# Performance work log

Hardware: AMD Instinct MI355X
Metric: run time of the kernel (lower is better)

Reference implementation:

```python
import jax, jax.numpy as jnp
import numpy as np

TEMP = 13.544
EPS = 1e-5  # BatchNorm2d default eps


def setup_inputs() -> dict:
    key = jax.random.key(0)
    k1, = jax.random.split(key, 1)
    N, S, E = 16, 1024, 512
    x = jax.random.normal(k1, (N, S, E), dtype=jnp.float32)
    gamma = jnp.ones((1,), dtype=jnp.float32)   # BatchNorm2d(1).weight
    beta = jnp.zeros((1,), dtype=jnp.float32)   # BatchNorm2d(1).bias
    return {"x": x, "gamma": gamma, "beta": beta}


def reference(x, gamma, beta):
    # Pairwise squared L2 distances via GEMM identity:
    # ||a-b||^2 = ||a||^2 + ||b||^2 - 2 a.b   (symmetric, matches the
    # original broadcast diff+square+sum without the O(S^2 E) intermediate)
    sq = jnp.sum(x * x, axis=-1)                    # (N, S)
    gram = jnp.einsum('bse,bte->bst', x, x)         # (N, S, S)
    d = sq[:, :, None] + sq[:, None, :] - 2.0 * gram  # (N, S, S)
    d = jnp.maximum(d, 0.0)                          # numerical floor (exact math is >= 0)

    # BatchNorm2d(1) in training mode: stats over all elements of the single channel
    d = d[:, None, :, :]                             # (N, 1, S, S)
    mean = jnp.mean(d)
    var = jnp.mean((d - mean) ** 2)                  # biased variance, as torch uses for normalization
    d_hat = (d - mean) * jax.lax.rsqrt(var + EPS)
    out = d_hat * gamma.reshape(1, 1, 1, 1) + beta.reshape(1, 1, 1, 1)

    # softmax(-out / 13.544) over last dim
    return jax.nn.softmax(-out / TEMP, axis=-1)      # (N, 1, S, S)
```

## Files before the change

kernel.cpp:

```cpp
#include <hip/hip_runtime.h>
#include <hip/hip_bf16.h>


#define S_DIM 1024
#define E_DIM 512
#define NBATCH 16
#define NSTEP (E_DIM / 32)
#define TEMP_C 13.544

typedef __attribute__((ext_vector_type(4))) float f32x4;
typedef __attribute__((ext_vector_type(8))) short bf16x8;
typedef __attribute__((ext_vector_type(8))) _Float16 f16x8;

__device__ inline unsigned pkbf(float lo, float hi) {
  unsigned a = __float_as_uint(lo), b = __float_as_uint(hi);
  a = (a + 0x7FFFu + ((a >> 16) & 1u)) >> 16;
  b = (b + 0x7FFFu + ((b >> 16) & 1u)) & 0xFFFF0000u;
  return b | a;
}

__device__ inline void gload16(const void* g, void* l) {
  __builtin_amdgcn_global_load_lds(
      (const __attribute__((address_space(1))) unsigned*)g,
      (__attribute__((address_space(3))) unsigned*)l, 16, 0, 0);
}

__global__ __launch_bounds__(256) void sqcvt(const float* __restrict__ x,
                                             ushort* __restrict__ xb16,
                                             float* __restrict__ sq,
                                             double* __restrict__ sums) {
  const int wave = threadIdx.x >> 6, lane = threadIdx.x & 63;
  const size_t row = (size_t)blockIdx.x * 4 + wave;
  const float4* xr = reinterpret_cast<const float4*>(x + row * E_DIM);
  float4 a = xr[lane * 2], b = xr[lane * 2 + 1];
  uint4 p;
  p.x = pkbf(a.x, a.y); p.y = pkbf(a.z, a.w);
  p.z = pkbf(b.x, b.y); p.w = pkbf(b.z, b.w);
  *reinterpret_cast<uint4*>(xb16 + row * E_DIM + lane * 8) = p;
  float s = a.x*a.x + a.y*a.y + a.z*a.z + a.w*a.w +
            b.x*b.x + b.y*b.y + b.z*b.z + b.w*b.w;
#pragma unroll
  for (int o = 32; o > 0; o >>= 1) s += __shfl_xor(s, o);
  if (lane == 0) sq[row] = s;
  if (blockIdx.x == 0 && threadIdx.x == 0) { sums[0] = 0.0; sums[1] = 0.0; }
}

template <int MODE>
__global__ __launch_bounds__(512, 2) void gram5(const ushort* __restrict__ xb16,
                                                const float* __restrict__ sq,
                                                float* __restrict__ dout,
                                                _Float16* __restrict__ dp,
                                                double* __restrict__ sums) {
  __shared__ ushort lA[3][8192];
  __shared__ ushort lB[3][8192];
  __shared__ double red[16];

  const int tid = threadIdx.x, wave = tid >> 6, lane = tid & 63;
  const int wr = wave >> 2, wc = wave & 3;

  const int bid = blockIdx.x;
  const int xcd = bid & 7, j = bid >> 3;
  const int b = xcd * 2 + (j >> 4);
  const int tile = j & 15;
  const int tr = tile >> 2, tc = tile & 3;

  const ushort* xb = xb16 + (size_t)b * (S_DIM * E_DIM);
  const int rowA0 = tr * 256, rowB0 = tc * 256;

  int eA[2], eB[2];
#pragma unroll
  for (int i = 0; i < 2; ++i) {
    int p = i * 512 + tid;
    int r = p >> 2;
    int s = (p & 3) ^ ((r >> 1) & 3);
    eA[i] = (rowA0 + r) * E_DIM + s * 8;
    eB[i] = (rowB0 + r) * E_DIM + s * 8;
  }

  auto stage = [&](int buf, int k0) {
    char* la = (char*)&lA[buf][0];
    char* lb = (char*)&lB[buf][0];
    gload16(xb + eA[0] + k0, la + (wave * 64 + lane) * 16);
    gload16(xb + eA[1] + k0, la + 8192 + (wave * 64 + lane) * 16);
    gload16(xb + eB[0] + k0, lb + (wave * 64 + lane) * 16);
    gload16(xb + eB[1] + k0, lb + 8192 + (wave * 64 + lane) * 16);
  };

  f32x4 acc[8][4] = {};

  stage(0, 0);
  stage(1, 32);
  int cur = 0;
#pragma unroll 1
  for (int ks = 0; ks < NSTEP; ++ks) {
    if (ks < NSTEP - 1) {
      asm volatile("s_waitcnt vmcnt(4)" ::: "memory");
    } else {
      asm volatile("s_waitcnt vmcnt(0)" ::: "memory");
    }
    __builtin_amdgcn_s_barrier();
    __builtin_amdgcn_sched_barrier(0);
    if (ks + 2 < NSTEP) {
      int nb = cur + 2; if (nb >= 3) nb -= 3;
      stage(nb, (ks + 2) * 32);
    }
    __builtin_amdgcn_sched_barrier(0);

    bf16x8 af[8], bfr[4];
    const int s0 = lane >> 4;
    const char* la = (const char*)&lA[cur][0];
    const char* lb = (const char*)&lB[cur][0];
#pragma unroll
    for (int m = 0; m < 8; ++m) {
      int row = wr * 128 + m * 16 + (lane & 15);
      af[m] = *reinterpret_cast<const bf16x8*>(la + row * 64 + ((s0 ^ ((row >> 1) & 3)) << 4));
    }
#pragma unroll
    for (int n = 0; n < 4; ++n) {
      int row = wc * 64 + n * 16 + (lane & 15);
      bfr[n] = *reinterpret_cast<const bf16x8*>(lb + row * 64 + ((s0 ^ ((row >> 1) & 3)) << 4));
    }
#pragma unroll
    for (int m = 0; m < 8; ++m)
#pragma unroll
      for (int n = 0; n < 4; ++n)
        acc[m][n] = __builtin_amdgcn_mfma_f32_16x16x32_bf16(af[m], bfr[n], acc[m][n], 0, 0, 0);

    if (++cur >= 3) cur = 0;
  }

  const float* sqb = sq + b * S_DIM;
  double sd = 0.0, sd2 = 0.0;
#pragma unroll
  for (int m = 0; m < 8; ++m) {
    int gr0 = tr * 256 + wr * 128 + m * 16 + ((lane >> 4) << 2);
    float sqr0 = sqb[gr0], sqr1 = sqb[gr0 + 1], sqr2 = sqb[gr0 + 2], sqr3 = sqb[gr0 + 3];
#pragma unroll
    for (int n = 0; n < 4; ++n) {
      int gc = tc * 256 + wc * 64 + n * 16 + (lane & 15);
      float sqc = sqb[gc];
      float d0 = fmaxf(sqr0 + sqc - 2.0f * acc[m][n][0], 0.0f);
      float d1 = fmaxf(sqr1 + sqc - 2.0f * acc[m][n][1], 0.0f);
      float d2 = fmaxf(sqr2 + sqc - 2.0f * acc[m][n][2], 0.0f);
      float d3 = fmaxf(sqr3 + sqc - 2.0f * acc[m][n][3], 0.0f);
      if (MODE == 0) {
        float* dbase = dout + (size_t)b * S_DIM * S_DIM;
        dbase[(size_t)(gr0 + 0) * S_DIM + gc] = d0;
        dbase[(size_t)(gr0 + 1) * S_DIM + gc] = d1;
        dbase[(size_t)(gr0 + 2) * S_DIM + gc] = d2;
        dbase[(size_t)(gr0 + 3) * S_DIM + gc] = d3;
      } else {
        _Float16* dbase = dp + (size_t)b * S_DIM * S_DIM;
        dbase[(size_t)(gr0 + 0) * S_DIM + gc] = (_Float16)(d0 - sqr0);
        dbase[(size_t)(gr0 + 1) * S_DIM + gc] = (_Float16)(d1 - sqr1);
        dbase[(size_t)(gr0 + 2) * S_DIM + gc] = (_Float16)(d2 - sqr2);
        dbase[(size_t)(gr0 + 3) * S_DIM + gc] = (_Float16)(d3 - sqr3);
      }
      sd += (double)d0 + (double)d1 + (double)d2 + (double)d3;
      sd2 += (double)d0 * d0 + (double)d1 * d1 + (double)d2 * d2 + (double)d3 * d3;
    }
  }
#pragma unroll
  for (int o = 32; o > 0; o >>= 1) {
    sd += __shfl_xor(sd, o);
    sd2 += __shfl_xor(sd2, o);
  }
  if (lane == 0) { red[wave] = sd; red[8 + wave] = sd2; }
  __syncthreads();
  if (tid == 0) {
    double t1 = 0.0, t2 = 0.0;
#pragma unroll
    for (int w = 0; w < 8; ++w) { t1 += red[w]; t2 += red[8 + w]; }
    atomicAdd(&sums[0], t1);
    atomicAdd(&sums[1], t2);
  }
}

__device__ inline float ln_scale(const double* sums, const float* gamma) {
  constexpr double invN = 1.0 / (16.0 * 1024.0 * 1024.0);
  double mean = sums[0] * invN;
  double var = sums[1] * invN - mean * mean;
  return (float)(-((double)gamma[0]) / (sqrt(var + 1e-5) * TEMP_C));
}

__global__ __launch_bounds__(256) void softmax_f32(float* __restrict__ d,
                                                   const double* __restrict__ sums,
                                                   const float* __restrict__ gamma) {
  const int wave = threadIdx.x >> 6, lane = threadIdx.x & 63;
  const size_t row = (size_t)blockIdx.x * 4 + wave;
  const float scale = ln_scale(sums, gamma);
  float4* r4 = reinterpret_cast<float4*>(d + row * S_DIM);
  float4 v[4];
#pragma unroll
  for (int i = 0; i < 4; ++i) v[i] = r4[lane + 64 * i];
  float l[16];
#pragma unroll
  for (int i = 0; i < 4; ++i) {
    l[4*i+0] = scale * v[i].x; l[4*i+1] = scale * v[i].y;
    l[4*i+2] = scale * v[i].z; l[4*i+3] = scale * v[i].w;
  }
  float mx = l[0];
#pragma unroll
  for (int i = 1; i < 16; ++i) mx = fmaxf(mx, l[i]);
#pragma unroll
  for (int o = 32; o > 0; o >>= 1) mx = fmaxf(mx, __shfl_xor(mx, o));
  const float L2E = 1.4426950408889634f;
  float e[16], s = 0.f;
#pragma unroll
  for (int i = 0; i < 16; ++i) { e[i] = exp2f((l[i] - mx) * L2E); s += e[i]; }
#pragma unroll
  for (int o = 32; o > 0; o >>= 1) s += __shfl_xor(s, o);
  float inv = 1.0f / s;
#pragma unroll
  for (int i = 0; i < 4; ++i)
    r4[lane + 64 * i] = make_float4(e[4*i]*inv, e[4*i+1]*inv, e[4*i+2]*inv, e[4*i+3]*inv);
}

__global__ __launch_bounds__(256) void softmax_f16(const _Float16* __restrict__ dp,
                                                   float* __restrict__ out,
                                                   const double* __restrict__ sums,
                                                   const float* __restrict__ gamma) {
  const int wave = threadIdx.x >> 6, lane = threadIdx.x & 63;
  const size_t row = (size_t)blockIdx.x * 4 + wave;
  const float scale = ln_scale(sums, gamma);
  const f16x8* r8 = reinterpret_cast<const f16x8*>(dp + row * S_DIM);
  f16x8 h0 = r8[lane * 2], h1 = r8[lane * 2 + 1];
  float l[16];
#pragma unroll
  for (int i = 0; i < 8; ++i) { l[i] = scale * (float)h0[i]; l[8 + i] = scale * (float)h1[i]; }
  float mx = l[0];
#pragma unroll
  for (int i = 1; i < 16; ++i) mx = fmaxf(mx, l[i]);
#pragma unroll
  for (int o = 32; o > 0; o >>= 1) mx = fmaxf(mx, __shfl_xor(mx, o));
  const float L2E = 1.4426950408889634f;
  float e[16], s = 0.f;
#pragma unroll
  for (int i = 0; i < 16; ++i) { e[i] = exp2f((l[i] - mx) * L2E); s += e[i]; }
#pragma unroll
  for (int o = 32; o > 0; o >>= 1) s += __shfl_xor(s, o);
  float inv = 1.0f / s;
  float4* o4 = reinterpret_cast<float4*>(out + row * S_DIM);
#pragma unroll
  for (int i = 0; i < 4; ++i)
    o4[lane * 4 + i] = make_float4(e[4*i]*inv, e[4*i+1]*inv, e[4*i+2]*inv, e[4*i+3]*inv);
}

extern "C" void kernel_launch(void* const* d_in, const int* in_sizes, int n_in,
                              void* d_out, int out_size, void* d_ws, size_t ws_size,
                              hipStream_t stream) {
  const float* x = (const float*)d_in[0];
  const float* gamma = (const float*)d_in[1];
  float* out = (float*)d_out;
  double* sums = (double*)d_ws;
  float* sq = (float*)((char*)d_ws + 256);
  ushort* xb16 = (ushort*)((char*)d_ws + 256 + 65536);
  _Float16* dp = (_Float16*)((char*)d_ws + 256 + 65536 +
                             (size_t)NBATCH * S_DIM * E_DIM * 2);
  const size_t need_b = 256 + 65536 + (size_t)NBATCH * S_DIM * E_DIM * 2;
  const size_t need_a = need_b + (size_t)NBATCH * S_DIM * S_DIM * 2;

  sqcvt<<<dim3(NBATCH * S_DIM / 4), dim3(256), 0, stream>>>(x, xb16, sq, sums);
  if (ws_size >= need_a) {
    gram5<1><<<dim3(256), dim3(512), 0, stream>>>(xb16, sq, out, dp, sums);
    softmax_f16<<<dim3(NBATCH * S_DIM / 4), dim3(256), 0, stream>>>(dp, out, sums, gamma);
  } else {
    gram5<0><<<dim3(256), dim3(512), 0, stream>>>(xb16, sq, out, dp, sums);
    softmax_f32<<<dim3(NBATCH * S_DIM / 4), dim3(256), 0, stream>>>(out, sums, gamma);
  }
}
```

Baseline: 144.4 us.

## Switch GEMM pipeline to double-buffered 64-wide K steps with one barrier

The Gram-matrix kernel drops its triple-buffered LDS pipeline over 32-wide K slices, which used manual vmcnt waits. It now double-buffers 64-wide K slices, each held as two 32-wide sub-chunks. Each iteration issues the next slice's global-to-LDS loads after a single __syncthreads and runs two MFMA sub-steps. The aim is to halve the number of barriers and loop iterations. The cost is a prefetch distance of only one step and more LDS per block (128KB versus 96KB). Correctness relies on the compiler inserting the vmcnt waits for the LDS-DMA loads before the barrier.

```diff
diff --git a/kernel.cpp b/kernel.cpp
--- a/kernel.cpp
+++ b/kernel.cpp
@@ -5,7 +5,7 @@
 #define S_DIM 1024
 #define E_DIM 512
 #define NBATCH 16
-#define NSTEP (E_DIM / 32)
+#define NSTEP2 (E_DIM / 64)
 #define TEMP_C 13.544
 
 typedef __attribute__((ext_vector_type(4))) float f32x4;
@@ -46,13 +46,13 @@
 }
 
 template <int MODE>
-__global__ __launch_bounds__(512, 2) void gram5(const ushort* __restrict__ xb16,
+__global__ __launch_bounds__(512, 2) void gram6(const ushort* __restrict__ xb16,
                                                 const float* __restrict__ sq,
                                                 float* __restrict__ dout,
                                                 _Float16* __restrict__ dp,
                                                 double* __restrict__ sums) {
-  __shared__ ushort lA[3][8192];
-  __shared__ ushort lB[3][8192];
+  __shared__ ushort lA[2][2][8192];
+  __shared__ ushort lB[2][2][8192];
   __shared__ double red[16];
 
   const int tid = threadIdx.x, wave = tid >> 6, lane = tid & 63;
@@ -78,55 +78,48 @@
   }
 
   auto stage = [&](int buf, int k0) {
-    char* la = (char*)&lA[buf][0];
-    char* lb = (char*)&lB[buf][0];
-    gload16(xb + eA[0] + k0, la + (wave * 64 + lane) * 16);
-    gload16(xb + eA[1] + k0, la + 8192 + (wave * 64 + lane) * 16);
-    gload16(xb + eB[0] + k0, lb + (wave * 64 + lane) * 16);
-    gload16(xb + eB[1] + k0, lb + 8192 + (wave * 64 + lane) * 16);
+#pragma unroll
+    for (int c = 0; c < 2; ++c) {
+      char* la = (char*)&lA[buf][c][0];
+      char* lb = (char*)&lB[buf][c][0];
+      gload16(xb + eA[0] + k0 + c * 32, la + tid * 16);
+      gload16(xb + eA[1] + k0 + c * 32, la + 8192 + tid * 16);
+      gload16(xb + eB[0] + k0 + c * 32, lb + tid * 16);
+      gload16(xb + eB[1] + k0 + c * 32, lb + 8192 + tid * 16);
+    }
   };
 
   f32x4 acc[8][4] = {};
 
   stage(0, 0);
-  stage(1, 32);
-  int cur = 0;
+  int buf = 0;
 #pragma unroll 1
-  for (int ks = 0; ks < NSTEP; ++ks) {
-    if (ks < NSTEP - 1) {
-      asm volatile("s_waitcnt vmcnt(4)" ::: "memory");
-    } else {
-      asm volatile("s_waitcnt vmcnt(0)" ::: "memory");
+  for (int ks = 0; ks < NSTEP2; ++ks) {
+    __syncthreads();
+    if (ks + 1 < NSTEP2) stage(buf ^ 1, (ks + 1) * 64);
+#pragma unroll
+    for (int c = 0; c < 2; ++c) {
+      bf16x8 af[8], bfr[4];
+      const int s0 = lane >> 4;
+      const char* la = (const char*)&lA[buf][c][0];
+      const char* lb = (const char*)&lB[buf][c][0];
+#pragma unroll
+      for (int m = 0; m < 8; ++m) {
+        int row = wr * 128 + m * 16 + (lane & 15);
+        af[m] = *reinterpret_cast<const bf16x8*>(la + row * 64 + ((s0 ^ ((row >> 1) & 3)) << 4));
+      }
+#pragma unroll
+      for (int n = 0; n < 4; ++n) {
+        int row = wc * 64 + n * 16 + (lane & 15);
+        bfr[n] = *reinterpret_cast<const bf16x8*>(lb + row * 64 + ((s0 ^ ((row >> 1) & 3)) << 4));
+      }
+#pragma unroll
+      for (int m = 0; m < 8; ++m)
+#pragma unroll
+        for (int n = 0; n < 4; ++n)
+          acc[m][n] = __builtin_amdgcn_mfma_f32_16x16x32_bf16(af[m], bfr[n], acc[m][n], 0, 0, 0);
     }
-    __builtin_amdgcn_s_barrier();
-    __builtin_amdgcn_sched_barrier(0);
-    if (ks + 2 < NSTEP) {
-      int nb = cur + 2; if (nb >= 3) nb -= 3;
-      stage(nb, (ks + 2) * 32);
-    }
-    __builtin_amdgcn_sched_barrier(0);
-
-    bf16x8 af[8], bfr[4];
-    const int s0 = lane >> 4;
-    const char* la = (const char*)&lA[cur][0];
-    const char* lb = (const char*)&lB[cur][0];
-#pragma unroll
-    for (int m = 0; m < 8; ++m) {
-      int row = wr * 128 + m * 16 + (lane & 15);
-      af[m] = *reinterpret_cast<const bf16x8*>(la + row * 64 + ((s0 ^ ((row >> 1) & 3)) << 4));
-    }
-#pragma unroll
-    for (int n = 0; n < 4; ++n) {
-      int row = wc * 64 + n * 16 + (lane & 15);
-      bfr[n] = *reinterpret_cast<const bf16x8*>(lb + row * 64 + ((s0 ^ ((row >> 1) & 3)) << 4));
-    }
-#pragma unroll
-    for (int m = 0; m < 8; ++m)
-#pragma unroll
-      for (int n = 0; n < 4; ++n)
-        acc[m][n] = __builtin_amdgcn_mfma_f32_16x16x32_bf16(af[m], bfr[n], acc[m][n], 0, 0, 0);
-
-    if (++cur >= 3) cur = 0;
+    buf ^= 1;
   }
 
   const float* sqb = sq + b * S_DIM;
@@ -262,10 +255,10 @@
 
   sqcvt<<<dim3(NBATCH * S_DIM / 4), dim3(256), 0, stream>>>(x, xb16, sq, sums);
   if (ws_size >= need_a) {
-    gram5<1><<<dim3(256), dim3(512), 0, stream>>>(xb16, sq, out, dp, sums);
+    gram6<1><<<dim3(256), dim3(512), 0, stream>>>(xb16, sq, out, dp, sums);
     softmax_f16<<<dim3(NBATCH * S_DIM / 4), dim3(256), 0, stream>>>(dp, out, sums, gamma);
   } else {
-    gram5<0><<<dim3(256), dim3(512), 0, stream>>>(xb16, sq, out, dp, sums);
+    gram6<0><<<dim3(256), dim3(512), 0, stream>>>(xb16, sq, out, dp, sums);
     softmax_f32<<<dim3(NBATCH * S_DIM / 4), dim3(256), 0, stream>>>(out, sums, gamma);
   }
 }
```

New measurement: 143.3 us. About the same (-0.8%).
